# Kernel tuning notes

Hardware: AMD Instinct MI355X
Metric: run time of the kernel (lower is better)

## Reference

```python
import jax, jax.numpy as jnp
import numpy as np

N_EMBD = 2048
N_HEAD = 16
N_KV_HEAD = 4
HEAD_DIM = 128
KV_REPEATS = N_HEAD // N_KV_HEAD
ROPE_THETA = 10000.0


def rotate_half(x):
    # interleaved pair rotation: (x0,x1,x2,x3,...) -> (-x1,x0,-x3,x2,...)
    x_even = x[..., 0::2]
    x_odd = x[..., 1::2]
    return jnp.stack((-x_odd, x_even), axis=-1).reshape(x.shape)


def apply_rope(q, k, position_ids):
    inv_freq = 1.0 / (ROPE_THETA ** (jnp.arange(0, HEAD_DIM, 2, dtype=jnp.float32) / HEAD_DIM))
    freqs = position_ids.astype(jnp.float32)[:, None] * inv_freq[None, :]  # [S, D/2]
    emb = jnp.repeat(freqs, 2, axis=-1)  # [S, D] interleaved
    cos = jnp.cos(emb)[None, None, :, :]
    sin = jnp.sin(emb)[None, None, :, :]
    return q * cos + rotate_half(q) * sin, k * cos + rotate_half(k) * sin


def setup_inputs() -> dict:
    key = jax.random.key(0)
    ks = jax.random.split(key, 5)
    B, S = 2, 2048
    x = jax.random.normal(ks[0], (B, S, N_EMBD), dtype=jnp.float32)
    position_ids = jnp.arange(S, dtype=jnp.int32)
    scale = 0.02
    Wq = jax.random.normal(ks[1], (N_HEAD * HEAD_DIM, N_EMBD), dtype=jnp.float32) * scale
    Wk = jax.random.normal(ks[2], (N_KV_HEAD * HEAD_DIM, N_EMBD), dtype=jnp.float32) * scale
    Wv = jax.random.normal(ks[3], (N_KV_HEAD * HEAD_DIM, N_EMBD), dtype=jnp.float32) * scale
    Wo = jax.random.normal(ks[4], (N_EMBD, N_EMBD), dtype=jnp.float32) * scale
    return {"x": x, "Wq": Wq, "Wk": Wk, "Wv": Wv, "Wo": Wo, "position_ids": position_ids}


def reference(x, Wq, Wk, Wv, Wo, position_ids):
    B, S, _ = x.shape
    q = (x @ Wq.T).reshape(B, S, N_HEAD, HEAD_DIM).transpose(0, 2, 1, 3)      # [B,H,S,D]
    k = (x @ Wk.T).reshape(B, S, N_KV_HEAD, HEAD_DIM).transpose(0, 2, 1, 3)  # [B,Hkv,S,D]
    v = (x @ Wv.T).reshape(B, S, N_KV_HEAD, HEAD_DIM).transpose(0, 2, 1, 3)
    q, k = apply_rope(q, k, position_ids)
    # GQA: repeat kv heads consecutively
    k = jnp.repeat(k, KV_REPEATS, axis=1)  # [B,H,S,D]
    v = jnp.repeat(v, KV_REPEATS, axis=1)
    scores = jnp.einsum('bhqd,bhkd->bhqk', q, k) / jnp.sqrt(jnp.asarray(HEAD_DIM, q.dtype))
    key_positions = jnp.arange(S)
    mask = key_positions[None, :] > position_ids[:, None]  # [S, S]
    scores = jnp.where(mask[None, None, :, :], jnp.finfo(scores.dtype).min, scores)
    weights = jax.nn.softmax(scores.astype(jnp.float32), axis=-1).astype(q.dtype)
    y = jnp.einsum('bhqk,bhkd->bhqd', weights, v)
    y = y.transpose(0, 2, 1, 3).reshape(B, S, N_EMBD)
    return y @ Wo.T
```

## Files before the change

### kernel.cpp

```cpp
#include <hip/hip_runtime.h>
#include <stdint.h>

typedef unsigned short u16;
typedef unsigned int   u32;
typedef __attribute__((ext_vector_type(8))) short short8;
typedef __attribute__((ext_vector_type(4))) float f32x4;

#define S_LEN 2048
#define NEMB  2048
#define NH    16
#define NKV   4
#define HD    128
#define BATCH 2
#define MROWS (BATCH*S_LEN)

#define SCALE_Q 0.12751744f

__device__ __forceinline__ u16 f2bf(float f){
  u32 u = __float_as_uint(f);
  u += 0x7fffu + ((u>>16)&1u);
  return (u16)(u>>16);
}
__device__ __forceinline__ float bf2f(u16 h){
  return __uint_as_float(((u32)h)<<16);
}
__device__ __forceinline__ float exp2_fast(float x){
  float r;
  asm("v_exp_f32 %0, %1" : "=v"(r) : "v"(x));
  return r;
}

typedef __attribute__((address_space(1))) const void gc_void;
typedef __attribute__((address_space(3))) void lds_void;
__device__ __forceinline__ void load_lds16(const void* g, void* l){
  __builtin_amdgcn_global_load_lds((gc_void*)(uintptr_t)g,
      (lds_void*)(u32)(uintptr_t)l, 16, 0, 0);
}

__global__ __launch_bounds__(256) void convert_kernel(
    const float* __restrict__ x, const float* __restrict__ wq,
    const float* __restrict__ wk, const float* __restrict__ wv,
    const float* __restrict__ wo,
    u16* __restrict__ xb, u16* __restrict__ wcb, u16* __restrict__ wob){
  const size_t NX=2097152, NWQ=1048576, NWK=262144, NWV=262144, NWO=1048576;
  const size_t total = NX+NWQ+NWK+NWV+NWO;
  for (size_t i = (size_t)blockIdx.x*blockDim.x + threadIdx.x; i < total;
       i += (size_t)gridDim.x*blockDim.x){
    const float* src; u16* dst; size_t j = i;
    if (j < NX){ src=x; dst=xb; }
    else { j-=NX;
      if (j<NWQ){ src=wq; dst=wcb; }
      else { j-=NWQ;
        if (j<NWK){ src=wk; dst=wcb+4194304; }
        else { j-=NWK;
          if (j<NWV){ src=wv; dst=wcb+5242880; }
          else { j-=NWV; src=wo; dst=wob; } } } }
    float4 v = *(const float4*)(src + j*4);
    u32 lo = (u32)f2bf(v.x) | ((u32)f2bf(v.y)<<16);
    u32 hi = (u32)f2bf(v.z) | ((u32)f2bf(v.w)<<16);
    uint2 pk; pk.x = lo; pk.y = hi;
    *(uint2*)(dst + j*4) = pk;
  }
}

__global__ __launch_bounds__(256) void rope_table_kernel(const int* __restrict__ pos,
                                                         float2* __restrict__ tab){
  int id = blockIdx.x*256 + threadIdx.x;
  if (id >= S_LEN*64) return;
  int s = id >> 6, i = id & 63;
  float p = (float)pos[s];
  float inv = __expf(-((float)(2*i)) * (1.0f/128.0f) * 9.210340371976184f);
  float f = p * inv;
  float sv, cv;
  sincosf(f, &sv, &cv);
  tab[id] = make_float2(cv, sv);
}

__global__ __launch_bounds__(256) void transpose_v_kernel(const u16* __restrict__ vb,
                                                          u16* __restrict__ vt){
  __shared__ u16 tl[64][72];
  int bx = blockIdx.x;
  int m0 = (bx & 63)*64;
  int d0 = (bx >> 6)*64;
  int tid = threadIdx.x;
  #pragma unroll
  for (int i=0;i<2;i++){
    int t16 = i*256 + tid;
    int sl = t16 >> 3, dc = t16 & 7;
    *(uint4*)&tl[sl][dc*8] = *(const uint4*)&vb[(size_t)(m0+sl)*512 + d0 + dc*8];
  }
  __syncthreads();
  #pragma unroll
  for (int i=0;i<2;i++){
    int t16 = i*256 + tid;
    int sch = t16 >> 6, dl = t16 & 63;
    union { uint4 v; u16 e[8]; } O;
    #pragma unroll
    for (int j=0;j<8;j++) O.e[j] = tl[sch*8+j][dl];
    *(uint4*)&vt[(size_t)(d0+dl)*4096 + m0 + sch*8] = O.v;
  }
}

template<int EPI>
__global__ __launch_bounds__(256,2) void gemm128_kernel(
    const u16* __restrict__ A, const u16* __restrict__ B, int K,
    const float2* __restrict__ tab,
    u16* __restrict__ q_out, u16* __restrict__ k_out, u16* __restrict__ v_out,
    float* __restrict__ f_out){
  __shared__ u16 sA[2][128*32];
  __shared__ u16 sB[2][128*32];
  int tid = threadIdx.x;
  int wave = tid >> 6, lane = tid & 63;
  int lr = lane & 15, lc = lane >> 4;
  int wm = (wave>>1)*64, wn = (wave&1)*64;
  int bm = blockIdx.y*128, bn = blockIdx.x*128;
  const u16* Ag = A + (size_t)bm*K;
  const u16* Bg = B + (size_t)bn*K;

  auto stage = [&](int buf, int kt){
    const u16* Ak = Ag + kt*32;
    const u16* Bk = Bg + kt*32;
    #pragma unroll
    for (int rrd=0; rrd<2; ++rrd){
      int t16 = rrd*256 + tid;
      int row = t16 >> 2, ch = t16 & 3;
      u16* lb = &sA[buf][(size_t)(rrd*256 + (tid & 192))*8];
      load_lds16(Ak + (size_t)row*K + ch*8, lb);
    }
    #pragma unroll
    for (int rrd=0; rrd<2; ++rrd){
      int t16 = rrd*256 + tid;
      int row = t16 >> 2, ch = t16 & 3;
      u16* lb = &sB[buf][(size_t)(rrd*256 + (tid & 192))*8];
      load_lds16(Bk + (size_t)row*K + ch*8, lb);
    }
  };

  f32x4 acc[4][4];
  #pragma unroll
  for (int i=0;i<4;i++)
    #pragma unroll
    for (int j=0;j<4;j++) acc[i][j] = (f32x4)0.0f;

  stage(0,0);
  __syncthreads();
  int nk = K >> 5;
  int cur = 0;
  for (int kt=0; kt<nk; ++kt){
    if (kt+1 < nk) stage(cur^1, kt+1);
    short8 af[4], bfr[4];
    #pragma unroll
    for (int i=0;i<4;i++){
      af[i]  = *(const short8*)&sA[cur][(wm + i*16 + lr)*32 + lc*8];
      bfr[i] = *(const short8*)&sB[cur][(wn + i*16 + lr)*32 + lc*8];
    }
    __builtin_amdgcn_s_setprio(1);
    #pragma unroll
    for (int i=0;i<4;i++)
      #pragma unroll
      for (int j=0;j<4;j++)
        acc[i][j] = __builtin_amdgcn_mfma_f32_16x16x32_bf16(af[i], bfr[j], acc[i][j], 0,0,0);
    __builtin_amdgcn_s_setprio(0);
    __syncthreads();
    cur ^= 1;
  }

  #pragma unroll
  for (int i=0;i<4;i++){
    #pragma unroll
    for (int j=0;j<4;j++){
      #pragma unroll
      for (int r=0;r<4;r++){
        int m = bm + wm + i*16 + lc*4 + r;
        int n = bn + wn + j*16 + lr;
        float v = acc[i][j][r];
        if (EPI == 0){
          float p = __shfl_xor(v, 1);
          if (n < 2048){
            float2 cs = tab[((m & (S_LEN-1))<<6) + ((n & 127)>>1)];
            float o = (n & 1) ? (v*cs.x + p*cs.y) : (v*cs.x - p*cs.y);
            q_out[(size_t)m*2048 + n] = f2bf(o * SCALE_Q);
          } else if (n < 2560){
            int d = n - 2048;
            float2 cs = tab[((m & (S_LEN-1))<<6) + ((d & 127)>>1)];
            float o = (n & 1) ? (v*cs.x + p*cs.y) : (v*cs.x - p*cs.y);
            k_out[(size_t)m*512 + d] = f2bf(o);
          } else {
            v_out[(size_t)m*512 + (n-2560)] = f2bf(v);
          }
        } else {
          f_out[(size_t)m*2048 + n] = v;
        }
      }
    }
  }
}

__global__ __launch_bounds__(256,2) void attn_kernel(
    const u16* __restrict__ Q, const u16* __restrict__ Kb,
    const u16* __restrict__ Vt, u16* __restrict__ Y){
  __shared__ u16 sK[2][64*128];
  __shared__ u16 sVt[2][128*64];
  __shared__ u16 sP[4][16*64];

  int tid = threadIdx.x, wave = tid>>6, lane = tid&63;
  int lr = lane&15, lc = lane>>4;

  int bid = blockIdx.x;
  int kvg  = bid & 7;
  int rest = bid >> 3;
  int pj   = rest & 15;
  int hsub = rest >> 4;
  int b  = kvg >> 2;
  int hk = kvg & 3;
  int h  = hk*4 + hsub;

  const u16* Kg = Kb + (size_t)(b*S_LEN)*512 + hk*HD;
  const u16* Vg = Vt + (size_t)(hk*HD)*4096 + b*S_LEN;

  auto stage = [&](int buf, int kv0){
    #pragma unroll
    for (int i=0;i<4;i++){
      int t16 = i*256 + tid;
      int row = t16 >> 4, c = t16 & 15;
      int cgl = c ^ (row & 7);
      load_lds16(Kg + (size_t)(kv0+row)*512 + cgl*8,
                 &sK[buf][(size_t)(i*256 + (tid & 192))*8]);
    }
    #pragma unroll
    for (int i=0;i<4;i++){
      int t16 = i*256 + tid;
      int d = t16 >> 3, c = t16 & 7;
      int cgl = c ^ (d & 7);
      load_lds16(Vg + (size_t)d*4096 + kv0 + cgl*8,
                 &sVt[buf][(size_t)(i*256 + (tid & 192))*8]);
    }
  };

  char* spb = (char*)sP[wave];

  #pragma unroll 1
  for (int pass=0; pass<2; ++pass){
    int qt  = pass ? pj : (31 - pj);
    int q0  = qt*64;
    int qrb = q0 + wave*16;
    const u16* Qg = Q + (size_t)(b*S_LEN + qrb)*NEMB + h*HD;

    short8 qf[4];
    #pragma unroll
    for (int c=0;c<4;c++)
      qf[c] = *(const short8*)&Qg[(size_t)lr*NEMB + c*32 + lc*8];

    float m_run[4], l_run[4];
    #pragma unroll
    for (int r=0;r<4;r++){ m_run[r]=-1e30f; l_run[r]=0.0f; }
    f32x4 o[8];
    #pragma unroll
    for (int i=0;i<8;i++) o[i]=(f32x4)0.0f;

    int nt = qt + 1;
    stage(0,0);
    __syncthreads();
    int cur=0;
    for (int t=0;t<nt;++t){
      int kv0 = t*64;
      if (t+1<nt) stage(cur^1,(t+1)*64);

      f32x4 sc[4];
      #pragma unroll
      for (int c2=0;c2<4;c2++) sc[c2]=(f32x4)0.0f;
      const char* skb = (const char*)sK[cur];
      __builtin_amdgcn_s_setprio(1);
      #pragma unroll
      for (int c2=0;c2<4;c2++){
        int rr = c2*16 + lr;
        int xo = (rr&7)<<4;
        #pragma unroll
        for (int c=0;c<4;c++){
          int byteoff = (rr*256 + c*64 + lc*16) ^ xo;
          short8 kf = *(const short8*)(skb + byteoff);
          sc[c2] = __builtin_amdgcn_mfma_f32_16x16x32_bf16(qf[c], kf, sc[c2], 0,0,0);
        }
      }
      __builtin_amdgcn_s_setprio(0);

      if (t == nt-1){
        #pragma unroll
        for (int c2=0;c2<4;c2++){
          int kvgl = kv0 + c2*16 + lr;
          #pragma unroll
          for (int r=0;r<4;r++){
            int qg = qrb + lc*4 + r;
            if (kvgl > qg) sc[c2][r] = -1e30f;
          }
        }
      }

      float lmax[4];
      bool need = false;
      #pragma unroll
      for (int r=0;r<4;r++){
        lmax[r] = fmaxf(fmaxf(sc[0][r],sc[1][r]), fmaxf(sc[2][r],sc[3][r]));
        need = need || (lmax[r] > m_run[r] + 8.0f);
      }
      if (__any(need)){
        float fac[4];
        #pragma unroll
        for (int r=0;r<4;r++){
          float mm = lmax[r];
          mm = fmaxf(mm, __shfl_xor(mm,1));
          mm = fmaxf(mm, __shfl_xor(mm,2));
          mm = fmaxf(mm, __shfl_xor(mm,4));
          mm = fmaxf(mm, __shfl_xor(mm,8));
          float mn = fmaxf(m_run[r], mm);
          fac[r] = exp2_fast(m_run[r]-mn);
          m_run[r] = mn;
          l_run[r] *= fac[r];
        }
        #pragma unroll
        for (int i=0;i<8;i++)
          #pragma unroll
          for (int r=0;r<4;r++) o[i][r] *= fac[r];
      }
      #pragma unroll
      for (int r=0;r<4;r++){
        float p0 = exp2_fast(sc[0][r]-m_run[r]);
        float p1 = exp2_fast(sc[1][r]-m_run[r]);
        float p2 = exp2_fast(sc[2][r]-m_run[r]);
        float p3 = exp2_fast(sc[3][r]-m_run[r]);
        sc[0][r]=p0; sc[1][r]=p1; sc[2][r]=p2; sc[3][r]=p3;
        float ss = (p0+p1)+(p2+p3);
        ss += __shfl_xor(ss,1); ss += __shfl_xor(ss,2);
        ss += __shfl_xor(ss,4); ss += __shfl_xor(ss,8);
        l_run[r] += ss;
      }

      #pragma unroll
      for (int c2=0;c2<4;c2++){
        #pragma unroll
        for (int r=0;r<4;r++){
          int row = lc*4+r;
          int byteoff = (row*128 + (c2*16+lr)*2) ^ ((row&7)<<4);
          *(u16*)(spb + byteoff) = f2bf(sc[c2][r]);
        }
      }
      short8 pa[2];
      {
        int xop = (lr&7)<<4;
        pa[0] = *(const short8*)(spb + ((lr*128 + lc*16) ^ xop));
        pa[1] = *(const short8*)(spb + ((lr*128 + 64 + lc*16) ^ xop));
      }

      const char* svb = (const char*)sVt[cur];
      __builtin_amdgcn_s_setprio(1);
      #pragma unroll
      for (int n=0;n<8;n++){
        int d = n*16+lr;
        int xo = (d&7)<<4;
        #pragma unroll
        for (int ks=0;ks<2;ks++){
          int byteoff = (d*128 + ks*64 + lc*16) ^ xo;
          short8 vf = *(const short8*)(svb + byteoff);
          o[n] = __builtin_amdgcn_mfma_f32_16x16x32_bf16(pa[ks], vf, o[n], 0,0,0);
        }
      }
      __builtin_amdgcn_s_setprio(0);

      __syncthreads();
      cur ^= 1;
    }

    u16* Yg = Y + (size_t)(b*S_LEN + qrb)*NEMB + h*HD;
    #pragma unroll
    for (int n=0;n<8;n++){
      #pragma unroll
      for (int r=0;r<4;r++){
        float v = o[n][r] / l_run[r];
        Yg[(size_t)(lc*4+r)*NEMB + n*16 + lr] = f2bf(v);
      }
    }
    __syncthreads();
  }
}

extern "C" void kernel_launch(void* const* d_in, const int* in_sizes, int n_in,
                              void* d_out, int out_size, void* d_ws, size_t ws_size,
                              hipStream_t stream){
  const float* x  = (const float*)d_in[0];
  const float* wq = (const float*)d_in[1];
  const float* wk = (const float*)d_in[2];
  const float* wv = (const float*)d_in[3];
  const float* wo = (const float*)d_in[4];
  const int*  pos = (const int*)d_in[5];
  float* out = (float*)d_out;

  char* ws = (char*)d_ws;
  size_t off = 0;
  auto alloc = [&](size_t bytes)->char*{
    char* p = ws + off; off += (bytes + 255) & ~(size_t)255; return p;
  };
  u16* xb  = (u16*)alloc(8388608ull*2);
  u16* wcb = (u16*)alloc(6291456ull*2);
  u16* wob = (u16*)alloc(4194304ull*2);
  u16* qb  = (u16*)alloc(8388608ull*2);
  u16* kb  = (u16*)alloc(2097152ull*2);
  u16* vb  = (u16*)alloc(2097152ull*2);
  u16* yb  = (u16*)alloc(8388608ull*2);
  float2* tab = (float2*)alloc((size_t)S_LEN*64*8);
  u16* vt = xb;

  convert_kernel<<<2048,256,0,stream>>>(x,wq,wk,wv,wo,xb,wcb,wob);
  rope_table_kernel<<<512,256,0,stream>>>(pos, tab);
  gemm128_kernel<0><<<dim3(24,32),256,0,stream>>>(xb, wcb, 2048, tab, qb, kb, vb, nullptr);
  transpose_v_kernel<<<512,256,0,stream>>>(vb, vt);
  attn_kernel<<<512,256,0,stream>>>(qb, kb, vt, yb);
  gemm128_kernel<1><<<dim3(16,32),256,0,stream>>>(yb, wob, 2048, nullptr, nullptr,nullptr,nullptr, out);
}
```

Measured before the change: 314.2 us.

## Fuse rope table into convert, swizzle GEMM blocks, defer softmax row-sum reduction

```diff
diff --git a/kernel.cpp b/kernel.cpp
--- a/kernel.cpp
+++ b/kernel.cpp
@@ -21,6 +21,9 @@
   u += 0x7fffu + ((u>>16)&1u);
   return (u16)(u>>16);
 }
+__device__ __forceinline__ u16 f2bf_t(float f){
+  return (u16)(__float_as_uint(f)>>16);
+}
 __device__ __forceinline__ float bf2f(u16 h){
   return __uint_as_float(((u32)h)<<16);
 }
@@ -41,7 +44,8 @@
     const float* __restrict__ x, const float* __restrict__ wq,
     const float* __restrict__ wk, const float* __restrict__ wv,
     const float* __restrict__ wo,
-    u16* __restrict__ xb, u16* __restrict__ wcb, u16* __restrict__ wob){
+    u16* __restrict__ xb, u16* __restrict__ wcb, u16* __restrict__ wob,
+    const int* __restrict__ pos, float2* __restrict__ tab){
   const size_t NX=2097152, NWQ=1048576, NWK=262144, NWV=262144, NWO=1048576;
   const size_t total = NX+NWQ+NWK+NWV+NWO;
   for (size_t i = (size_t)blockIdx.x*blockDim.x + threadIdx.x; i < total;
@@ -61,19 +65,16 @@
     uint2 pk; pk.x = lo; pk.y = hi;
     *(uint2*)(dst + j*4) = pk;
   }
-}
-
-__global__ __launch_bounds__(256) void rope_table_kernel(const int* __restrict__ pos,
-                                                         float2* __restrict__ tab){
-  int id = blockIdx.x*256 + threadIdx.x;
-  if (id >= S_LEN*64) return;
-  int s = id >> 6, i = id & 63;
-  float p = (float)pos[s];
-  float inv = __expf(-((float)(2*i)) * (1.0f/128.0f) * 9.210340371976184f);
-  float f = p * inv;
-  float sv, cv;
-  sincosf(f, &sv, &cv);
-  tab[id] = make_float2(cv, sv);
+  for (int id = blockIdx.x*blockDim.x + threadIdx.x; id < S_LEN*64;
+       id += gridDim.x*blockDim.x){
+    int s = id >> 6, i = id & 63;
+    float p = (float)pos[s];
+    float inv = __expf(-((float)(2*i)) * (1.0f/128.0f) * 9.210340371976184f);
+    float f = p * inv;
+    float sv, cv;
+    sincosf(f, &sv, &cv);
+    tab[id] = make_float2(cv, sv);
+  }
 }
 
 __global__ __launch_bounds__(256) void transpose_v_kernel(const u16* __restrict__ vb,
@@ -102,7 +103,7 @@
 }
 
 template<int EPI>
-__global__ __launch_bounds__(256,2) void gemm128_kernel(
+__global__ __launch_bounds__(256,3) void gemm128_kernel(
     const u16* __restrict__ A, const u16* __restrict__ B, int K,
     const float2* __restrict__ tab,
     u16* __restrict__ q_out, u16* __restrict__ k_out, u16* __restrict__ v_out,
@@ -113,7 +114,13 @@
   int wave = tid >> 6, lane = tid & 63;
   int lr = lane & 15, lc = lane >> 4;
   int wm = (wave>>1)*64, wn = (wave&1)*64;
-  int bm = blockIdx.y*128, bn = blockIdx.x*128;
+
+  int nwgx = gridDim.x;
+  int nwg  = nwgx * gridDim.y;
+  int wg   = blockIdx.y*nwgx + blockIdx.x;
+  wg = (wg & 7)*(nwg >> 3) + (wg >> 3);
+  int bm = (wg / nwgx)*128, bn = (wg % nwgx)*128;
+
   const u16* Ag = A + (size_t)bm*K;
   const u16* Bg = B + (size_t)bn*K;
 
@@ -329,10 +336,7 @@
         float p2 = exp2_fast(sc[2][r]-m_run[r]);
         float p3 = exp2_fast(sc[3][r]-m_run[r]);
         sc[0][r]=p0; sc[1][r]=p1; sc[2][r]=p2; sc[3][r]=p3;
-        float ss = (p0+p1)+(p2+p3);
-        ss += __shfl_xor(ss,1); ss += __shfl_xor(ss,2);
-        ss += __shfl_xor(ss,4); ss += __shfl_xor(ss,8);
-        l_run[r] += ss;
+        l_run[r] += (p0+p1)+(p2+p3);
       }
 
       #pragma unroll
@@ -341,7 +345,7 @@
         for (int r=0;r<4;r++){
           int row = lc*4+r;
           int byteoff = (row*128 + (c2*16+lr)*2) ^ ((row&7)<<4);
-          *(u16*)(spb + byteoff) = f2bf(sc[c2][r]);
+          *(u16*)(spb + byteoff) = f2bf_t(sc[c2][r]);
         }
       }
       short8 pa[2];
@@ -370,12 +374,20 @@
       cur ^= 1;
     }
 
+    float inv[4];
+    #pragma unroll
+    for (int r=0;r<4;r++){
+      float s = l_run[r];
+      s += __shfl_xor(s,1); s += __shfl_xor(s,2);
+      s += __shfl_xor(s,4); s += __shfl_xor(s,8);
+      inv[r] = __builtin_amdgcn_rcpf(s);
+    }
     u16* Yg = Y + (size_t)(b*S_LEN + qrb)*NEMB + h*HD;
     #pragma unroll
     for (int n=0;n<8;n++){
       #pragma unroll
       for (int r=0;r<4;r++){
-        float v = o[n][r] / l_run[r];
+        float v = o[n][r] * inv[r];
         Yg[(size_t)(lc*4+r)*NEMB + n*16 + lr] = f2bf(v);
       }
     }
@@ -409,8 +421,7 @@
   float2* tab = (float2*)alloc((size_t)S_LEN*64*8);
   u16* vt = xb;
 
-  convert_kernel<<<2048,256,0,stream>>>(x,wq,wk,wv,wo,xb,wcb,wob);
-  rope_table_kernel<<<512,256,0,stream>>>(pos, tab);
+  convert_kernel<<<2048,256,0,stream>>>(x,wq,wk,wv,wo,xb,wcb,wob,pos,tab);
   gemm128_kernel<0><<<dim3(24,32),256,0,stream>>>(xb, wcb, 2048, tab, qb, kb, vb, nullptr);
   transpose_v_kernel<<<512,256,0,stream>>>(vb, vt);
   attn_kernel<<<512,256,0,stream>>>(qb, kb, vt, yb);
```

Result: faster. 292.8 us (-6.8%).
